# Kernel optimization log

Hardware: AMD Instinct MI355X
Metric: run time of the kernel (lower is better)

Reference implementation:

```python
import jax, jax.numpy as jnp
import numpy as np

D = 128          # embed_dim
NSYM = 100000    # num_symbols
PAD = NSYM       # padding idx (zero row)
B = 2048         # query batch
FEW = 5          # support set size
M = 128          # max neighbors
KTAB = 64        # knn table width
K = 32           # knn_k topk
STEPS = 4        # process_steps
DM = 2 * D       # d_model for encoders (256)
HID = 2 * DM     # LSTM hidden (512)


def _cos(a, b):
    # torch F.cosine_similarity, eps=1e-8; a [B,1,d], b [B,N,d] -> [B,N]
    num = jnp.sum(a * b, axis=-1)
    den = jnp.maximum(jnp.linalg.norm(a, axis=-1) * jnp.linalg.norm(b, axis=-1), 1e-8)
    return num / den


def _l2n(x):
    return x / jnp.maximum(jnp.linalg.norm(x, axis=-1, keepdims=True), 1e-12)


def _neighbor_encoder(conn, ids, knn_tab, emb, gcn_w, gcn_w_b, gcn_b, gate_w, gate_b):
    rel = emb[conn[..., 0]]                      # [N,M,D]
    ent = emb[conn[..., 1]]                      # [N,M,D]
    center = emb[ids][:, None, :]                # [N,1,D]
    sim = _cos(center, ent)                      # [N,M]
    _, idx = jax.lax.top_k(sim, K)               # [N,K]
    rel_k = jnp.take_along_axis(rel, idx[..., None], axis=1)
    ent_k = jnp.take_along_axis(ent, idx[..., None], axis=1)
    h = jnp.concatenate([rel_k, ent_k], axis=-1) @ gcn_w.T + gcn_w_b + gcn_b
    struct = jnp.tanh(h.mean(axis=1))            # [N,D]
    # knn branch: gather knn neighbor ids, cosine topk, pad-relation embeds (zero row)
    kent = emb[knn_tab[ids]]                     # [N,KTAB,D]
    sim2 = _cos(center, kent)
    _, idx2 = jax.lax.top_k(sim2, K)
    kent_k = jnp.take_along_axis(kent, idx2[..., None], axis=1)
    pad_row = jax.lax.stop_gradient(emb[PAD])    # padding_idx row (zeros, no grad)
    krel = jnp.broadcast_to(pad_row, kent_k.shape)
    h2 = jnp.concatenate([krel, kent_k], axis=-1) @ gcn_w.T + gcn_w_b + gcn_b
    knn_mean = jnp.tanh(h2.mean(axis=1))         # [N,D]
    alpha = jax.nn.sigmoid(jnp.concatenate([struct, knn_mean], axis=-1) @ gate_w.T + gate_b)
    return (1.0 - alpha) * struct + alpha * knn_mean


def _support_encoder(x, p1_w, p1_b, p2_w, p2_b, ln_g, ln_b):
    o = jax.nn.relu(x @ p1_w.T + p1_b) @ p2_w.T + p2_b
    z = o + x
    mu = z.mean(axis=-1, keepdims=True)
    sig = z.std(axis=-1, ddof=1, keepdims=True)  # torch unbiased std
    return (z - mu) / (sig + 1e-3) * ln_g + ln_b


def _query_encoder(support, query, w_ih, w_hh, b_ih, b_hh):
    # attLSTM processing block; support [1,DM], query [B,DM]
    n = query.shape[0]
    h_r = jnp.zeros((n, HID), query.dtype)
    c = jnp.zeros((n, HID), query.dtype)
    h = query
    for _ in range(STEPS):
        g = query @ w_ih.T + b_ih + h_r @ w_hh.T + b_hh
        i, f, gg, o = jnp.split(g, 4, axis=-1)
        c = jax.nn.sigmoid(f) * c + jax.nn.sigmoid(i) * jnp.tanh(gg)
        h_ = jax.nn.sigmoid(o) * jnp.tanh(c)
        h = query + h_[:, :DM]
        attn = jax.nn.softmax(h @ support.T, axis=1)  # [B,1]
        r = attn @ support                             # [B,DM]
        h_r = jnp.concatenate([h, r], axis=1)
    return h


def _forward(query, support, q_l_conn, q_r_conn, s_l_conn, s_r_conn, knn_neighbors,
             emb, gcn_w, gcn_w_b, gcn_b, gate_w, gate_b,
             p1_w, p1_b, p2_w, p2_b, ln_g, ln_b, w_ih, w_hh, b_ih, b_hh):
    ne = lambda conn, ids: _neighbor_encoder(conn, ids, knn_neighbors, emb,
                                             gcn_w, gcn_w_b, gcn_b, gate_w, gate_b)
    ql = ne(q_l_conn, query[:, 0])
    qr = ne(q_r_conn, query[:, 1])
    sl = ne(s_l_conn, support[:, 0])
    sr = ne(s_r_conn, support[:, 1])
    qn = jnp.concatenate([ql, qr], axis=-1)   # [B,DM]
    sn = jnp.concatenate([sl, sr], axis=-1)   # [FEW,DM]
    se = lambda x: _support_encoder(x, p1_w, p1_b, p2_w, p2_b, ln_g, ln_b)
    support_g = se(sn).mean(axis=0, keepdims=True)  # [1,DM]
    query_g = se(qn)                                 # [B,DM]
    query_f = _l2n(_query_encoder(support_g, query_g, w_ih, w_hh, b_ih, b_hh))
    sg = _l2n(support_g[0])
    return query_f @ sg                              # [B]


def setup_inputs() -> dict:
    key = jax.random.key(0)
    ks = jax.random.split(key, 24)
    f = lambda i, shape, s=0.05: jax.random.normal(ks[i], shape, dtype=jnp.float32) * s
    ri = lambda i, shape: jax.random.randint(ks[i], shape, 0, NSYM).astype(jnp.int32)
    emb = f(0, (NSYM + 1, D), 0.5).at[PAD].set(0.0)
    return dict(
        query=ri(1, (B, 2)), support=ri(2, (FEW, 2)),
        q_l_conn=ri(3, (B, M, 2)),
        q_l_deg=jax.random.randint(ks[4], (B,), 1, M).astype(jnp.int32),
        q_r_conn=ri(5, (B, M, 2)),
        q_r_deg=jax.random.randint(ks[6], (B,), 1, M).astype(jnp.int32),
        s_l_conn=ri(7, (FEW, M, 2)),
        s_l_deg=jax.random.randint(ks[8], (FEW,), 1, M).astype(jnp.int32),
        s_r_conn=ri(9, (FEW, M, 2)),
        s_r_deg=jax.random.randint(ks[10], (FEW,), 1, M).astype(jnp.int32),
        knn_neighbors=ri(11, (NSYM + 1, KTAB)),
        emb=emb,
        gcn_w=f(12, (D, 2 * D)), gcn_w_b=f(13, (D,)),
        gcn_b=jnp.zeros((D,), jnp.float32),
        gate_w=f(14, (1, 2 * D)), gate_b=jnp.zeros((1,), jnp.float32),
        p1_w=f(15, (2 * DM, DM)), p1_b=f(16, (2 * DM,)),
        p2_w=f(17, (DM, 2 * DM)), p2_b=f(18, (DM,)),
        ln_g=jnp.ones((DM,), jnp.float32), ln_b=jnp.zeros((DM,), jnp.float32),
        w_ih=f(19, (4 * HID, DM)), w_hh=f(20, (4 * HID, HID)),
        b_ih=f(21, (4 * HID,)), b_hh=f(22, (4 * HID,)),
    )


def reference(query, support, q_l_conn, q_l_deg, q_r_conn, q_r_deg,
              s_l_conn, s_l_deg, s_r_conn, s_r_deg, knn_neighbors,
              emb, gcn_w, gcn_w_b, gcn_b, gate_w, gate_b,
              p1_w, p1_b, p2_w, p2_b, ln_g, ln_b, w_ih, w_hh, b_ih, b_hh):
    # degrees are computed-but-unused in this fork's neighbor_encoder (plain mean)
    return _forward(query, support, q_l_conn, q_r_conn, s_l_conn, s_r_conn, knn_neighbors,
                    emb, gcn_w, gcn_w_b, gcn_b, gate_w, gate_b,
                    p1_w, p1_b, p2_w, p2_b, ln_g, ln_b, w_ih, w_hh, b_ih, b_hh)
```

## Files before the change

kernel.cpp:

```cpp
#include <hip/hip_runtime.h>
#include <hip/hip_bf16.h>

typedef unsigned short u16;
typedef unsigned int u32;

constexpr int ED   = 128;
constexpr int MC   = 128;
constexpr int KT   = 64;
constexpr int KS   = 32;
constexpr int NB   = 2048;
constexpr int NF   = 5;
constexpr int DMM  = 256;
constexpr int NG   = 1024;
constexpr int PADID = 100000;
constexpr int NROWS = 2*NB + 2*NF;
constexpr int MT   = (NROWS + 63)/64;
constexpr int MP   = MT*64;

typedef __attribute__((ext_vector_type(8))) short short8;
typedef __attribute__((ext_vector_type(4))) float floatx4;

__device__ __forceinline__ float bf2f(u16 u){
  union { u32 i; float f; } v; v.i = ((u32)u) << 16; return v.f;
}
__device__ __forceinline__ float lo2f(u32 w){
  union { u32 i; float f; } v; v.i = w << 16; return v.f;
}
__device__ __forceinline__ float hi2f(u32 w){
  union { u32 i; float f; } v; v.i = w & 0xffff0000u; return v.f;
}
__device__ __forceinline__ u16 f2bf(float f){
  union { float f; u32 i; } v; v.f = f;
  u32 r = v.i + 0x7FFFu + ((v.i >> 16) & 1u);
  return (u16)(r >> 16);
}
__device__ __forceinline__ float sigf(float x){ return 1.f / (1.f + expf(-x)); }

__device__ __forceinline__ float gld(const void* p, size_t i, bool bf){
  return bf ? bf2f(((const u16*)p)[i]) : ((const float*)p)[i];
}
__device__ __forceinline__ void ld2(const void* p, size_t i0, bool bf, float* o){
  if (bf){ u32 w = *(const u32*)((const u16*)p + i0); o[0]=lo2f(w); o[1]=hi2f(w); }
  else   { float2 v = *(const float2*)((const float*)p + i0); o[0]=v.x; o[1]=v.y; }
}
__device__ __forceinline__ void ld4(const void* p, size_t i0, bool bf, float* o){
  if (bf){ uint2 w = *(const uint2*)((const u16*)p + i0);
           o[0]=lo2f(w.x); o[1]=hi2f(w.x); o[2]=lo2f(w.y); o[3]=hi2f(w.y); }
  else   { float4 v = *(const float4*)((const float*)p + i0);
           o[0]=v.x; o[1]=v.y; o[2]=v.z; o[3]=v.w; }
}
__device__ __forceinline__ void ld8(const void* p, size_t i0, bool bf, float* o){
  if (bf){
    uint4 v = *(const uint4*)((const u16*)p + i0);
    o[0]=lo2f(v.x); o[1]=hi2f(v.x); o[2]=lo2f(v.y); o[3]=hi2f(v.y);
    o[4]=lo2f(v.z); o[5]=hi2f(v.z); o[6]=lo2f(v.w); o[7]=hi2f(v.w);
  } else {
    const float* f = (const float*)p + i0;
    float4 a = *(const float4*)f, b = *(const float4*)(f + 4);
    o[0]=a.x; o[1]=a.y; o[2]=a.z; o[3]=a.w; o[4]=b.x; o[5]=b.y; o[6]=b.z; o[7]=b.w;
  }
}
__device__ __forceinline__ float dotw(const void* w, size_t i0, const float* x, int n, bool bf){
  float acc = 0.f, t[8];
  #pragma unroll 4
  for (int j = 0; j < n; j += 8){
    ld8(w, i0 + j, bf, t);
    #pragma unroll
    for (int q = 0; q < 8; q++) acc += t[q]*x[j+q];
  }
  return acc;
}

__device__ __forceinline__ float waveSum(float v){
  #pragma unroll
  for (int o = 32; o > 0; o >>= 1) v += __shfl_xor(v, o, 64);
  return v;
}
__device__ __forceinline__ float blockSum(float v, float* s8){
  int lane = threadIdx.x & 63, wid = threadIdx.x >> 6;
  v = waveSum(v);
  __syncthreads();
  if (lane == 0) s8[wid] = v;
  __syncthreads();
  return s8[0] + s8[1] + s8[2] + s8[3];
}
__device__ __forceinline__ float2 blockSum2(float a, float b, float* s8){
  int lane = threadIdx.x & 63, wid = threadIdx.x >> 6;
  a = waveSum(a); b = waveSum(b);
  __syncthreads();
  if (lane == 0){ s8[wid] = a; s8[4 + wid] = b; }
  __syncthreads();
  float2 r;
  r.x = s8[0] + s8[1] + s8[2] + s8[3];
  r.y = s8[4] + s8[5] + s8[6] + s8[7];
  return r;
}

__global__ void sniff_kernel(const void* ln_g, int* flag){
  if (threadIdx.x == 0 && blockIdx.x == 0)
    *flag = (*(const u32*)ln_g == 0x3F803F80u) ? 1 : 0;
}

__global__ __launch_bounds__(256) void neighbor_kernel(
    const int* __restrict__ query, const int* __restrict__ support,
    const int* __restrict__ qlc, const int* __restrict__ qrc,
    const int* __restrict__ slc, const int* __restrict__ srcc,
    const int* __restrict__ knnt, const void* __restrict__ emb,
    float* __restrict__ gA, float* __restrict__ gK, const int* __restrict__ flag)
{
  const bool bf = (*flag != 0);
  int blk = blockIdx.x;
  const int* conn; int id;
  if (blk < NB)            { id = query[2*blk];                 conn = qlc + (size_t)blk*MC*2; }
  else if (blk < 2*NB)     { int r = blk - NB;   id = query[2*r+1];   conn = qrc + (size_t)r*MC*2; }
  else if (blk < 2*NB+NF)  { int r = blk - 2*NB; id = support[2*r];   conn = slc + (size_t)r*MC*2; }
  else                     { int r = blk - 2*NB - NF; id = support[2*r+1]; conn = srcc + (size_t)r*MC*2; }

  __shared__ float s_center[ED];
  __shared__ float s_sim[MC + KT];
  __shared__ float s_red[8];
  __shared__ int s_eid[MC + KT];
  __shared__ int s_selE[KS], s_selR[KS], s_selK[KS];
  __shared__ float s_mt[3][8][ED];

  const int tid = threadIdx.x, lane = tid & 63, wid = tid >> 6;

  if (tid < ED) s_center[tid] = gld(emb, (size_t)id*ED + tid, bf);
  if (tid < MC)           s_eid[tid] = conn[2*tid + 1];
  else if (tid < MC + KT) s_eid[tid] = knnt[(size_t)id*KT + (tid - MC)];

  float cpart = 0.f;
  if (tid < ED){ float c = s_center[tid]; cpart = c*c; }
  float cnorm = sqrtf(blockSum(cpart, s_red));

  const int g = lane & 15;
  float creg[8];
  #pragma unroll
  for (int j = 0; j < 8; j++) creg[j] = s_center[g*8 + j];

  #pragma unroll 4
  for (int m0 = wid*4; m0 < MC + KT; m0 += 16){
    int m = m0 + (lane >> 4);
    int eid = s_eid[m];
    float e[8];
    ld8(emb, (size_t)eid*ED + g*8, bf, e);
    float d = 0.f, q = 0.f;
    #pragma unroll
    for (int j = 0; j < 8; j++){ d += creg[j]*e[j]; q += e[j]*e[j]; }
    #pragma unroll
    for (int o = 8; o > 0; o >>= 1){ d += __shfl_xor(d, o, 64); q += __shfl_xor(q, o, 64); }
    if (g == 0) s_sim[m] = d / fmaxf(cnorm * sqrtf(q), 1e-8f);
  }
  __syncthreads();

  if (tid < MC){
    float v = s_sim[tid];
    int cnt = 0;
    #pragma unroll 8
    for (int j = 0; j < MC; j++){
      float w = s_sim[j];
      cnt += (w > v || (w == v && j < tid)) ? 1 : 0;
    }
    if (cnt < KS){ s_selR[cnt] = conn[2*tid]; s_selE[cnt] = s_eid[tid]; }
  } else if (tid < MC + KT){
    int t = tid - MC;
    float v = s_sim[MC + t];
    int cnt = 0;
    #pragma unroll 8
    for (int j = 0; j < KT; j++){
      float w = s_sim[MC + j];
      cnt += (w > v || (w == v && j < t)) ? 1 : 0;
    }
    if (cnt < KS) s_selK[cnt] = s_eid[MC + t];
  }
  __syncthreads();

  {
    const int slot = tid >> 5, c4 = (tid & 31)*4;
    float aR[4] = {0,0,0,0}, aE[4] = {0,0,0,0}, aK[4] = {0,0,0,0};
    #pragma unroll
    for (int k = 0; k < 4; k++){
      float t[4];
      ld4(emb, (size_t)s_selR[k*8 + slot]*ED + c4, bf, t);
      aR[0]+=t[0]; aR[1]+=t[1]; aR[2]+=t[2]; aR[3]+=t[3];
      ld4(emb, (size_t)s_selE[k*8 + slot]*ED + c4, bf, t);
      aE[0]+=t[0]; aE[1]+=t[1]; aE[2]+=t[2]; aE[3]+=t[3];
      ld4(emb, (size_t)s_selK[k*8 + slot]*ED + c4, bf, t);
      aK[0]+=t[0]; aK[1]+=t[1]; aK[2]+=t[2]; aK[3]+=t[3];
    }
    *(float4*)&s_mt[0][slot][c4] = make_float4(aR[0], aR[1], aR[2], aR[3]);
    *(float4*)&s_mt[1][slot][c4] = make_float4(aE[0], aE[1], aE[2], aE[3]);
    *(float4*)&s_mt[2][slot][c4] = make_float4(aK[0], aK[1], aK[2], aK[3]);
  }
  __syncthreads();
  {
    int dd = tid & (ED - 1), which = tid >> 7;
    float s = 0.f;
    #pragma unroll
    for (int p = 0; p < 8; p++) s += s_mt[which][p][dd];
    gA[(size_t)blk*DMM + which*ED + dd] = s * (1.f/KS);
    if (tid < ED){
      float sk = 0.f;
      #pragma unroll
      for (int p = 0; p < 8; p++) sk += s_mt[2][p][dd];
      gK[(size_t)blk*ED + dd] = sk * (1.f/KS);
    }
  }
}

__global__ __launch_bounds__(256) void gcn_gemm(
    const float* __restrict__ ARE, const float* __restrict__ AK,
    const void* __restrict__ gcn_w, const void* __restrict__ gcn_w_b,
    const void* __restrict__ gcn_b, float* __restrict__ C, const int* __restrict__ flag)
{
  const bool bf = (*flag != 0);
  __shared__ float As2[16][68];
  __shared__ float Ws2[16][68];
  int tid = threadIdx.x;
  int n0 = blockIdx.x * 64;
  int mt = blockIdx.y;
  const float* A; int lda, K, woff; size_t cbase; int mtt;
  if (mt < MT){ A = ARE; lda = DMM; K = DMM; woff = 0;  cbase = 0;              mtt = mt; }
  else        { A = AK;  lda = ED;  K = ED;  woff = ED; cbase = (size_t)MP*ED;  mtt = mt - MT; }
  int m0 = mtt*64;

  int tx = tid & 15, ty = tid >> 4;
  int sn_ = tid & 63, kq = tid >> 6;
  size_t wbase = (size_t)(n0 + sn_)*DMM + woff;
  int ar = tid >> 2, ac = (tid & 3)*4;
  const float* ap = A + (size_t)(m0 + ar)*lda + ac;

  float acc[4][4];
  #pragma unroll
  for (int i = 0; i < 4; i++)
    #pragma unroll
    for (int j = 0; j < 4; j++) acc[i][j] = 0.f;

  for (int kc = 0; kc < K; kc += 16){
    __syncthreads();
    float4 av = *(const float4*)(ap + kc);
    As2[ac+0][ar] = av.x; As2[ac+1][ar] = av.y; As2[ac+2][ar] = av.z; As2[ac+3][ar] = av.w;
    float wt[4];
    ld4(gcn_w, wbase + kc + kq*4, bf, wt);
    Ws2[kq*4+0][sn_] = wt[0]; Ws2[kq*4+1][sn_] = wt[1];
    Ws2[kq*4+2][sn_] = wt[2]; Ws2[kq*4+3][sn_] = wt[3];
    __syncthreads();
    #pragma unroll
    for (int k = 0; k < 16; k++){
      float4 a = *(const float4*)&As2[k][ty*4];
      float4 b = *(const float4*)&Ws2[k][tx*4];
      acc[0][0] += a.x*b.x; acc[0][1] += a.x*b.y; acc[0][2] += a.x*b.z; acc[0][3] += a.x*b.w;
      acc[1][0] += a.y*b.x; acc[1][1] += a.y*b.y; acc[1][2] += a.y*b.z; acc[1][3] += a.y*b.w;
      acc[2][0] += a.z*b.x; acc[2][1] += a.z*b.y; acc[2][2] += a.z*b.z; acc[2][3] += a.z*b.w;
      acc[3][0] += a.w*b.x; acc[3][1] += a.w*b.y; acc[3][2] += a.w*b.z; acc[3][3] += a.w*b.w;
    }
  }

  float b4[4];
  #pragma unroll
  for (int j = 0; j < 4; j++){
    int n = n0 + tx*4 + j;
    b4[j] = gld(gcn_w_b, n, bf) + gld(gcn_b, n, bf);
  }
  #pragma unroll
  for (int i = 0; i < 4; i++){
    int row = m0 + ty*4 + i;
    float4 v = make_float4(acc[i][0]+b4[0], acc[i][1]+b4[1], acc[i][2]+b4[2], acc[i][3]+b4[3]);
    *(float4*)(C + cbase + (size_t)row*ED + n0 + tx*4) = v;
  }
}

__global__ __launch_bounds__(256) void gcn_epilogue(
    const float* __restrict__ C, const void* __restrict__ gate_w,
    const void* __restrict__ gate_b, float* __restrict__ qn,
    float* __restrict__ sn, const int* __restrict__ flag)
{
  const bool bf = (*flag != 0);
  int wv = threadIdx.x >> 6, lane = threadIdx.x & 63;
  int r = blockIdx.x*4 + wv;
  if (r >= NROWS) return;
  const float* c1 = C + (size_t)r*ED;
  const float* c2 = C + (size_t)(MP + r)*ED;
  float2 sv = *(const float2*)(c1 + 2*lane);
  float2 kv = *(const float2*)(c2 + 2*lane);
  float s0 = tanhf(sv.x), s1 = tanhf(sv.y);
  float k0 = tanhf(kv.x), k1 = tanhf(kv.y);
  float gv = gld(gate_w, 2*lane, bf)*s0 + gld(gate_w, 2*lane+1, bf)*s1
           + gld(gate_w, ED + 2*lane, bf)*k0 + gld(gate_w, ED + 2*lane+1, bf)*k1;
  gv = waveSum(gv);
  float alpha = sigf(gv + gld(gate_b, 0, bf));
  float* outp;
  if (r < NB)             outp = qn + (size_t)r*DMM;
  else if (r < 2*NB)      outp = qn + (size_t)(r - NB)*DMM + ED;
  else if (r < 2*NB + NF) outp = sn + (size_t)(r - 2*NB)*DMM;
  else                    outp = sn + (size_t)(r - 2*NB - NF)*DMM + ED;
  float2 o;
  o.x = (1.f - alpha)*s0 + alpha*k0;
  o.y = (1.f - alpha)*s1 + alpha*k1;
  *(float2*)(outp + 2*lane) = o;
}

__global__ __launch_bounds__(256) void mlp_enc_kernel(
    const float* __restrict__ src,
    const void* __restrict__ p1_w, const void* __restrict__ p1_b,
    const void* __restrict__ p2_w, const void* __restrict__ p2_b,
    const void* __restrict__ ln_g, const void* __restrict__ ln_b,
    float* __restrict__ dst, int nrows, const int* __restrict__ flag)
{
  const bool bf = (*flag != 0);
  constexpr int RPB = 8;
  __shared__ float x[RPB][DMM];
  __shared__ float hid[RPB][2*DMM];
  __shared__ float s_red[8];
  int tid = threadIdx.x;
  int r0 = blockIdx.x * RPB;
  for (int r = 0; r < RPB; r++)
    x[r][tid] = (r0 + r < nrows) ? src[(size_t)(r0 + r)*DMM + tid] : 0.f;
  __syncthreads();

  {
    float acc0[RPB], acc1[RPB];
    #pragma unroll
    for (int r = 0; r < RPB; r++){ acc0[r] = 0.f; acc1[r] = 0.f; }
    for (int j8 = 0; j8 < DMM/8; j8++){
      float wa[8], wb[8];
      ld8(p1_w, (size_t)tid*DMM + j8*8, bf, wa);
      ld8(p1_w, (size_t)(tid+256)*DMM + j8*8, bf, wb);
      #pragma unroll
      for (int r = 0; r < RPB; r++){
        const float* xr = &x[r][j8*8];
        float s0 = 0.f, s1 = 0.f;
        #pragma unroll
        for (int q = 0; q < 8; q++){ float xv = xr[q]; s0 += wa[q]*xv; s1 += wb[q]*xv; }
        acc0[r] += s0; acc1[r] += s1;
      }
    }
    float bb0 = gld(p1_b, tid, bf), bb1 = gld(p1_b, tid + 256, bf);
    #pragma unroll
    for (int r = 0; r < RPB; r++){
      hid[r][tid]     = fmaxf(acc0[r] + bb0, 0.f);
      hid[r][tid+256] = fmaxf(acc1[r] + bb1, 0.f);
    }
  }
  __syncthreads();

  float zr[RPB];
  {
    #pragma unroll
    for (int r = 0; r < RPB; r++) zr[r] = 0.f;
    for (int j8 = 0; j8 < (2*DMM)/8; j8++){
      float wa[8];
      ld8(p2_w, (size_t)tid*(2*DMM) + j8*8, bf, wa);
      #pragma unroll
      for (int r = 0; r < RPB; r++){
        const float* hr = &hid[r][j8*8];
        float s0 = 0.f;
        #pragma unroll
        for (int q = 0; q < 8; q++) s0 += wa[q]*hr[q];
        zr[r] += s0;
      }
    }
    float bb = gld(p2_b, tid, bf);
    #pragma unroll
    for (int r = 0; r < RPB; r++) zr[r] += bb + x[r][tid];
  }

  float lg = gld(ln_g, tid, bf), lb = gld(ln_b, tid, bf);
  for (int r = 0; r < RPB; r++){
    float2 st = blockSum2(zr[r], zr[r]*zr[r], s_red);
    float mu = st.x * (1.f/DMM);
    float var = (st.y - (float)DMM*mu*mu) * (1.f/(DMM - 1));
    float sig = sqrtf(fmaxf(var, 0.f));
    if (r0 + r < nrows)
      dst[(size_t)(r0 + r)*DMM + tid] = (zr[r] - mu)/(sig + 1e-3f)*lg + lb;
  }
}

__global__ __launch_bounds__(256) void svec_kernel(
    const void* __restrict__ w_hh, const void* __restrict__ b_ih, const void* __restrict__ b_hh,
    const float* __restrict__ seS, float* __restrict__ cvec0, float* __restrict__ svec,
    float* __restrict__ sgn, const int* __restrict__ flag)
{
  const bool bf = (*flag != 0);
  __shared__ float sg[DMM];
  __shared__ float s_red[8];
  int tid = threadIdx.x;
  float a = 0.f;
  for (int r = 0; r < NF; r++) a += seS[r*DMM + tid];
  a *= (1.f/NF);
  sg[tid] = a;
  __syncthreads();
  if (blockIdx.x == 0){
    float nn = blockSum(a*a, s_red);
    sgn[tid] = a / fmaxf(sqrtf(nn), 1e-12f);
  }
  int u = blockIdx.x * 256 + tid;
  int wrow = (u >> 8)*512 + (u & 255);
  cvec0[u] = gld(b_ih, wrow, bf) + gld(b_hh, wrow, bf);
  svec[u] = dotw(w_hh, (size_t)wrow*(2*DMM) + DMM, sg, DMM, bf);
}

__global__ __launch_bounds__(256) void gemm_gates(
    const float* __restrict__ A,
    const void* __restrict__ W, int wstride,
    const float* __restrict__ addvec, const float* __restrict__ addmat,
    float* __restrict__ C, const int* __restrict__ flag)
{
  const bool bf = (*flag != 0);
  int tid = threadIdx.x;
  int n0 = blockIdx.x * 64, m0 = blockIdx.y * 64;

  if (bf){
    constexpr int KP = 136;
    __shared__ u16 As[64 * KP];
    __shared__ u16 Ws[64 * KP];
    const int wv = tid >> 6, lane = tid & 63;
    const int quad = lane >> 4, l16 = lane & 15;
    const int sr = tid >> 5, sc = tid & 31;

    floatx4 acc[4];
    #pragma unroll
    for (int t = 0; t < 4; t++) acc[t] = (floatx4){0.f, 0.f, 0.f, 0.f};

    for (int kc = 0; kc < 256; kc += 128){
      __syncthreads();
      #pragma unroll
      for (int i = 0; i < 8; i++){
        int r = i*8 + sr;
        float4 v = *(const float4*)(A + (size_t)(m0 + r)*256 + kc + sc*4);
        u32 p0 = (u32)f2bf(v.x) | ((u32)f2bf(v.y) << 16);
        u32 p1 = (u32)f2bf(v.z) | ((u32)f2bf(v.w) << 16);
        *(uint2*)&As[r*KP + sc*4] = make_uint2(p0, p1);
      }
      #pragma unroll
      for (int i = 0; i < 8; i++){
        int nn = i*8 + sr;
        int gn = n0 + nn;
        int wrow = (gn >> 8)*512 + (gn & 255);
        uint2 wv2 = *(const uint2*)((const u16*)W + (size_t)wrow*wstride + kc + sc*4);
        *(uint2*)&Ws[nn*KP + sc*4] = wv2;
      }
      __syncthreads();
      int am = wv*16 + l16;
      #pragma unroll
      for (int k1 = 0; k1 < 128; k1 += 32){
        int ko = k1 + quad*8;
        short8 af = *(const short8*)&As[am*KP + ko];
        #pragma unroll
        for (int t = 0; t < 4; t++){
          short8 bfr = *(const short8*)&Ws[(t*16 + l16)*KP + ko];
          acc[t] = __builtin_amdgcn_mfma_f32_16x16x32_bf16(af, bfr, acc[t], 0, 0, 0);
        }
      }
    }

    #pragma unroll
    for (int t = 0; t < 4; t++){
      int col = n0 + t*16 + l16;
      float av = addvec ? addvec[col] : 0.f;
      #pragma unroll
      for (int r = 0; r < 4; r++){
        int row = m0 + wv*16 + quad*4 + r;
        float val = acc[t][r] + av;
        if (addmat) val += addmat[(size_t)row*NG + col];
        C[(size_t)row*NG + col] = val;
      }
    }
    return;
  }

  {
    __shared__ float As2[16][68];
    __shared__ float Ws2[16][68];
    int tx = tid & 15, ty = tid >> 4;
    int sn_ = tid & 63, kq = tid >> 6;
    int gn = n0 + sn_;
    size_t wbase = (size_t)((gn >> 8)*512 + (gn & 255)) * wstride;
    int ar = tid >> 2, ac = (tid & 3) * 4;
    const float* ap = A + (size_t)(m0 + ar)*256 + ac;

    float acc[4][4];
    #pragma unroll
    for (int i = 0; i < 4; i++)
      #pragma unroll
      for (int j = 0; j < 4; j++) acc[i][j] = 0.f;

    for (int kc = 0; kc < 256; kc += 16){
      __syncthreads();
      float4 av = *(const float4*)(ap + kc);
      As2[ac+0][ar] = av.x; As2[ac+1][ar] = av.y; As2[ac+2][ar] = av.z; As2[ac+3][ar] = av.w;
      float wt[4];
      ld4(W, wbase + kc + kq*4, false, wt);
      Ws2[kq*4+0][sn_] = wt[0]; Ws2[kq*4+1][sn_] = wt[1];
      Ws2[kq*4+2][sn_] = wt[2]; Ws2[kq*4+3][sn_] = wt[3];
      __syncthreads();
      #pragma unroll
      for (int k = 0; k < 16; k++){
        float4 a = *(const float4*)&As2[k][ty*4];
        float4 b = *(const float4*)&Ws2[k][tx*4];
        acc[0][0] += a.x*b.x; acc[0][1] += a.x*b.y; acc[0][2] += a.x*b.z; acc[0][3] += a.x*b.w;
        acc[1][0] += a.y*b.x; acc[1][1] += a.y*b.y; acc[1][2] += a.y*b.z; acc[1][3] += a.y*b.w;
        acc[2][0] += a.z*b.x; acc[2][1] += a.z*b.y; acc[2][2] += a.z*b.z; acc[2][3] += a.z*b.w;
        acc[3][0] += a.w*b.x; acc[3][1] += a.w*b.y; acc[3][2] += a.w*b.z; acc[3][3] += a.w*b.w;
      }
    }

    float4 addc = make_float4(0.f, 0.f, 0.f, 0.f);
    if (addvec){
      float4 t = *(const float4*)(addvec + n0 + tx*4);
      addc.x = t.x; addc.y = t.y; addc.z = t.z; addc.w = t.w;
    }
    #pragma unroll
    for (int i = 0; i < 4; i++){
      int row = m0 + ty*4 + i;
      float4 v = make_float4(acc[i][0]+addc.x, acc[i][1]+addc.y, acc[i][2]+addc.z, acc[i][3]+addc.w);
      if (addmat){
        float4 t = *(const float4*)(addmat + (size_t)row*NG + n0 + tx*4);
        v.x += t.x; v.y += t.y; v.z += t.z; v.w += t.w;
      }
      *(float4*)(C + (size_t)row*NG + n0 + tx*4) = v;
    }
  }
}

__global__ __launch_bounds__(256) void lstm_elem(
    const float* __restrict__ g, const float* __restrict__ query_g,
    float* __restrict__ c, float* __restrict__ h, int first,
    const float* __restrict__ sgn, void* __restrict__ out, const int* __restrict__ flag)
{
  __shared__ float s_red[8];
  int b = blockIdx.x, j = threadIdx.x;
  const float* gb = g + (size_t)b*NG;
  float iv = gb[j], fv = gb[256 + j], gv = gb[512 + j], ov = gb[768 + j];
  float cc = first ? 0.f : c[(size_t)b*DMM + j];
  cc = sigf(fv)*cc + sigf(iv)*tanhf(gv);
  c[(size_t)b*DMM + j] = cc;
  float hh = query_g[(size_t)b*DMM + j] + sigf(ov)*tanhf(cc);
  h[(size_t)b*DMM + j] = hh;
  if (out){
    float2 st = blockSum2(hh*sgn[j], hh*hh, s_red);
    if (j == 0){
      float v = st.x / fmaxf(sqrtf(st.y), 1e-12f);
      if (*flag) ((__hip_bfloat16*)out)[b] = __float2bfloat16(v);
      else       ((float*)out)[b] = v;
    }
  }
}

extern "C" void kernel_launch(void* const* d_in, const int* in_sizes, int n_in,
                              void* d_out, int out_size, void* d_ws, size_t ws_size,
                              hipStream_t stream)
{
  const int* query   = (const int*)d_in[0];
  const int* support = (const int*)d_in[1];
  const int* qlc     = (const int*)d_in[2];
  const int* qrc     = (const int*)d_in[4];
  const int* slc     = (const int*)d_in[6];
  const int* srcc    = (const int*)d_in[8];
  const int* knnt    = (const int*)d_in[10];
  const void* emb     = d_in[11];
  const void* gcn_w   = d_in[12];
  const void* gcn_w_b = d_in[13];
  const void* gcn_b   = d_in[14];
  const void* gate_w  = d_in[15];
  const void* gate_b  = d_in[16];
  const void* p1_w    = d_in[17];
  const void* p1_b    = d_in[18];
  const void* p2_w    = d_in[19];
  const void* p2_b    = d_in[20];
  const void* ln_g    = d_in[21];
  const void* ln_b    = d_in[22];
  const void* w_ih    = d_in[23];
  const void* w_hh    = d_in[24];
  const void* b_ih    = d_in[25];
  const void* b_hh    = d_in[26];

  int* flag = (int*)d_ws;
  float* ws = (float*)d_ws + 64;
  size_t off = 0;
  float* qn        = ws + off; off += (size_t)NB*DMM;
  float* sn        = ws + off; off += NF*DMM;
  float* query_g   = ws + off; off += (size_t)NB*DMM;
  float* seS       = ws + off; off += NF*DMM;
  float* sgn       = ws + off; off += DMM;
  float* cvec0     = ws + off; off += NG;
  float* svec      = ws + off; off += NG;
  float* qx        = ws + off; off += (size_t)NB*NG;
  float* gbuf      = ws + off; off += (size_t)NB*NG;
  float* hbuf      = ws + off; off += (size_t)NB*DMM;
  float* cbuf      = ws + off; off += (size_t)NB*DMM;
  float* gA        = ws + off; off += (size_t)MP*DMM;
  float* gK        = ws + off; off += (size_t)MP*ED;
  float* gC        = ws + off; off += (size_t)2*MP*ED;
  (void)sn; (void)seS;

  sniff_kernel<<<1, 64, 0, stream>>>(ln_g, flag);

  neighbor_kernel<<<NROWS, 256, 0, stream>>>(
      query, support, qlc, qrc, slc, srcc, knnt, emb, gA, gK, flag);

  gcn_gemm<<<dim3(2, 2*MT), 256, 0, stream>>>(gA, gK, gcn_w, gcn_w_b, gcn_b, gC, flag);

  gcn_epilogue<<<(NROWS + 3)/4, 256, 0, stream>>>(gC, gate_w, gate_b, qn, sn, flag);

  mlp_enc_kernel<<<(NB + NF + 7)/8, 256, 0, stream>>>(
      qn, p1_w, p1_b, p2_w, p2_b, ln_g, ln_b, query_g, NB + NF, flag);

  svec_kernel<<<NG/256, 256, 0, stream>>>(w_hh, b_ih, b_hh, seS, cvec0, svec, sgn, flag);

  gemm_gates<<<dim3(NG/64, NB/64), 256, 0, stream>>>(query_g, w_ih, 256, cvec0, nullptr, qx, flag);

  lstm_elem<<<NB, 256, 0, stream>>>(qx, query_g, cbuf, hbuf, 1, nullptr, nullptr, flag);
  for (int s = 1; s < 4; s++){
    gemm_gates<<<dim3(NG/64, NB/64), 256, 0, stream>>>(hbuf, w_hh, 512, svec, qx, gbuf, flag);
    lstm_elem<<<NB, 256, 0, stream>>>(gbuf, query_g, cbuf, hbuf, 0,
                                      sgn, (s == 3) ? d_out : nullptr, flag);
  }

  (void)in_sizes; (void)n_in; (void)out_size; (void)ws_size;
}
```

Measured before the change: 434.1 us.

## Fuse LSTM steps into one persistent kernel with transposed fp32 weights

Replaces the per-step gate GEMM and elementwise LSTM launches with a single kernel. Each block keeps 8 rows of hidden and cell state in shared memory and registers across all four steps, reading fp32 weights that a prep kernel transposes first. This removes the round trips of the gate, h and c buffers through global memory and several kernel launches, and the separate sniff kernel is replaced by an inline dtype check in each kernel. In exchange the bf16 MFMA path is dropped for scalar fp32 FMAs, and each block re-reads the full weight matrices from cache.

```diff
diff --git a/kernel.cpp b/kernel.cpp
--- a/kernel.cpp
+++ b/kernel.cpp
@@ -17,9 +17,6 @@
 constexpr int MT   = (NROWS + 63)/64;
 constexpr int MP   = MT*64;
 
-typedef __attribute__((ext_vector_type(8))) short short8;
-typedef __attribute__((ext_vector_type(4))) float floatx4;
-
 __device__ __forceinline__ float bf2f(u16 u){
   union { u32 i; float f; } v; v.i = ((u32)u) << 16; return v.f;
 }
@@ -29,19 +26,14 @@
 __device__ __forceinline__ float hi2f(u32 w){
   union { u32 i; float f; } v; v.i = w & 0xffff0000u; return v.f;
 }
-__device__ __forceinline__ u16 f2bf(float f){
-  union { float f; u32 i; } v; v.f = f;
-  u32 r = v.i + 0x7FFFu + ((v.i >> 16) & 1u);
-  return (u16)(r >> 16);
-}
 __device__ __forceinline__ float sigf(float x){ return 1.f / (1.f + expf(-x)); }
+
+__device__ __forceinline__ bool sniff(const void* ln_g){
+  return *(const u32*)ln_g == 0x3F803F80u;
+}
 
 __device__ __forceinline__ float gld(const void* p, size_t i, bool bf){
   return bf ? bf2f(((const u16*)p)[i]) : ((const float*)p)[i];
-}
-__device__ __forceinline__ void ld2(const void* p, size_t i0, bool bf, float* o){
-  if (bf){ u32 w = *(const u32*)((const u16*)p + i0); o[0]=lo2f(w); o[1]=hi2f(w); }
-  else   { float2 v = *(const float2*)((const float*)p + i0); o[0]=v.x; o[1]=v.y; }
 }
 __device__ __forceinline__ void ld4(const void* p, size_t i0, bool bf, float* o){
   if (bf){ uint2 w = *(const uint2*)((const u16*)p + i0);
@@ -60,16 +52,6 @@
     o[0]=a.x; o[1]=a.y; o[2]=a.z; o[3]=a.w; o[4]=b.x; o[5]=b.y; o[6]=b.z; o[7]=b.w;
   }
 }
-__device__ __forceinline__ float dotw(const void* w, size_t i0, const float* x, int n, bool bf){
-  float acc = 0.f, t[8];
-  #pragma unroll 4
-  for (int j = 0; j < n; j += 8){
-    ld8(w, i0 + j, bf, t);
-    #pragma unroll
-    for (int q = 0; q < 8; q++) acc += t[q]*x[j+q];
-  }
-  return acc;
-}
 
 __device__ __forceinline__ float waveSum(float v){
   #pragma unroll
@@ -94,11 +76,6 @@
   r.x = s8[0] + s8[1] + s8[2] + s8[3];
   r.y = s8[4] + s8[5] + s8[6] + s8[7];
   return r;
-}
-
-__global__ void sniff_kernel(const void* ln_g, int* flag){
-  if (threadIdx.x == 0 && blockIdx.x == 0)
-    *flag = (*(const u32*)ln_g == 0x3F803F80u) ? 1 : 0;
 }
 
 __global__ __launch_bounds__(256) void neighbor_kernel(
@@ -106,9 +83,9 @@
     const int* __restrict__ qlc, const int* __restrict__ qrc,
     const int* __restrict__ slc, const int* __restrict__ srcc,
     const int* __restrict__ knnt, const void* __restrict__ emb,
-    float* __restrict__ gA, float* __restrict__ gK, const int* __restrict__ flag)
+    float* __restrict__ gA, float* __restrict__ gK, const void* __restrict__ ln_g)
 {
-  const bool bf = (*flag != 0);
+  const bool bf = sniff(ln_g);
   int blk = blockIdx.x;
   const int* conn; int id;
   if (blk < NB)            { id = query[2*blk];                 conn = qlc + (size_t)blk*MC*2; }
@@ -211,9 +188,9 @@
 __global__ __launch_bounds__(256) void gcn_gemm(
     const float* __restrict__ ARE, const float* __restrict__ AK,
     const void* __restrict__ gcn_w, const void* __restrict__ gcn_w_b,
-    const void* __restrict__ gcn_b, float* __restrict__ C, const int* __restrict__ flag)
+    const void* __restrict__ gcn_b, float* __restrict__ C, const void* __restrict__ ln_g)
 {
-  const bool bf = (*flag != 0);
+  const bool bf = sniff(ln_g);
   __shared__ float As2[16][68];
   __shared__ float Ws2[16][68];
   int tid = threadIdx.x;
@@ -273,9 +250,9 @@
 __global__ __launch_bounds__(256) void gcn_epilogue(
     const float* __restrict__ C, const void* __restrict__ gate_w,
     const void* __restrict__ gate_b, float* __restrict__ qn,
-    float* __restrict__ sn, const int* __restrict__ flag)
+    float* __restrict__ sn, const void* __restrict__ ln_g)
 {
-  const bool bf = (*flag != 0);
+  const bool bf = sniff(ln_g);
   int wv = threadIdx.x >> 6, lane = threadIdx.x & 63;
   int r = blockIdx.x*4 + wv;
   if (r >= NROWS) return;
@@ -305,9 +282,9 @@
     const void* __restrict__ p1_w, const void* __restrict__ p1_b,
     const void* __restrict__ p2_w, const void* __restrict__ p2_b,
     const void* __restrict__ ln_g, const void* __restrict__ ln_b,
-    float* __restrict__ dst, int nrows, const int* __restrict__ flag)
+    float* __restrict__ dst, int nrows)
 {
-  const bool bf = (*flag != 0);
+  const bool bf = sniff(ln_g);
   constexpr int RPB = 8;
   __shared__ float x[RPB][DMM];
   __shared__ float hid[RPB][2*DMM];
@@ -376,173 +353,229 @@
   }
 }
 
-__global__ __launch_bounds__(256) void svec_kernel(
-    const void* __restrict__ w_hh, const void* __restrict__ b_ih, const void* __restrict__ b_hh,
-    const float* __restrict__ seS, float* __restrict__ cvec0, float* __restrict__ svec,
-    float* __restrict__ sgn, const int* __restrict__ flag)
+__global__ __launch_bounds__(256) void prep_kernel(
+    const void* __restrict__ w_ih, const void* __restrict__ w_hh,
+    const void* __restrict__ b_ih, const void* __restrict__ b_hh,
+    const float* __restrict__ seS,
+    float* __restrict__ WT_ih, float* __restrict__ WT_hh,
+    float* __restrict__ svec, float* __restrict__ cvec0,
+    float* __restrict__ sgn, const void* __restrict__ ln_g)
 {
-  const bool bf = (*flag != 0);
-  __shared__ float sg[DMM];
-  __shared__ float s_red[8];
-  int tid = threadIdx.x;
-  float a = 0.f;
-  for (int r = 0; r < NF; r++) a += seS[r*DMM + tid];
-  a *= (1.f/NF);
-  sg[tid] = a;
-  __syncthreads();
-  if (blockIdx.x == 0){
-    float nn = blockSum(a*a, s_red);
-    sgn[tid] = a / fmaxf(sqrtf(nn), 1e-12f);
-  }
-  int u = blockIdx.x * 256 + tid;
-  int wrow = (u >> 8)*512 + (u & 255);
-  cvec0[u] = gld(b_ih, wrow, bf) + gld(b_hh, wrow, bf);
-  svec[u] = dotw(w_hh, (size_t)wrow*(2*DMM) + DMM, sg, DMM, bf);
-}
-
-__global__ __launch_bounds__(256) void gemm_gates(
-    const float* __restrict__ A,
-    const void* __restrict__ W, int wstride,
-    const float* __restrict__ addvec, const float* __restrict__ addmat,
-    float* __restrict__ C, const int* __restrict__ flag)
+  const bool bf = sniff(ln_g);
+  const int b = blockIdx.x, tid = threadIdx.x;
+  if (b < 32){
+    const void* W = (b < 16) ? w_ih : w_hh;
+    const int wstride = (b < 16) ? 256 : 512;
+    float* WT = (b < 16) ? WT_ih : WT_hh;
+    const int n0 = (b & 15) * 64;
+    __shared__ float tile[64][65];
+    const int nl = tid >> 2, kq = tid & 3;
+    const int kl = tid >> 2, nq = tid & 3;
+    const int wrow = ((n0 + nl) >> 8)*512 + ((n0 + nl) & 255);
+    for (int kc = 0; kc < 256; kc += 64){
+      __syncthreads();
+      float t[16];
+      ld8(W, (size_t)wrow*wstride + kc + kq*16,     bf, t);
+      ld8(W, (size_t)wrow*wstride + kc + kq*16 + 8, bf, t + 8);
+      #pragma unroll
+      for (int i = 0; i < 16; i++) tile[nl][kq*16 + i] = t[i];
+      __syncthreads();
+      float o[16];
+      #pragma unroll
+      for (int i = 0; i < 16; i++) o[i] = tile[nq*16 + i][kl];
+      #pragma unroll
+      for (int i = 0; i < 16; i += 4)
+        *(float4*)&WT[(size_t)(kc + kl)*NG + n0 + nq*16 + i] =
+            make_float4(o[i], o[i+1], o[i+2], o[i+3]);
+    }
+  } else {
+    const int n0 = (b - 32) * 64;
+    __shared__ float sg[DMM];
+    __shared__ float part[64][4];
+    __shared__ float s_red[8];
+    if (tid < DMM){
+      float a = 0.f;
+      #pragma unroll
+      for (int r = 0; r < NF; r++) a += seS[r*DMM + tid];
+      sg[tid] = a * (1.f/NF);
+    }
+    __syncthreads();
+    if (b == 32){
+      float sq = (tid < DMM) ? sg[tid]*sg[tid] : 0.f;
+      float nn = blockSum(sq, s_red);
+      if (tid < DMM) sgn[tid] = sg[tid] / fmaxf(sqrtf(nn), 1e-12f);
+    }
+    const int nl = tid >> 2, q = tid & 3;
+    const int n = n0 + nl;
+    const int wrow = (n >> 8)*512 + (n & 255);
+    float acc = 0.f, t[8];
+    #pragma unroll
+    for (int k8 = 0; k8 < 8; k8++){
+      ld8(w_hh, (size_t)wrow*(2*DMM) + DMM + q*64 + k8*8, bf, t);
+      #pragma unroll
+      for (int j = 0; j < 8; j++) acc += t[j]*sg[q*64 + k8*8 + j];
+    }
+    part[nl][q] = acc;
+    __syncthreads();
+    if (tid < 64){
+      svec[n0 + tid] = part[tid][0] + part[tid][1] + part[tid][2] + part[tid][3];
+      const int wr2 = ((n0 + tid) >> 8)*512 + ((n0 + tid) & 255);
+      cvec0[n0 + tid] = gld(b_ih, wr2, bf) + gld(b_hh, wr2, bf);
+    }
+  }
+}
+
+__global__ __launch_bounds__(256) void fused_lstm(
+    const float* __restrict__ query_g,
+    const float* __restrict__ WT_ih, const float* __restrict__ WT_hh,
+    const float* __restrict__ svec, const float* __restrict__ cvec0,
+    const float* __restrict__ sgn_g, const void* __restrict__ ln_g,
+    void* __restrict__ out)
 {
-  const bool bf = (*flag != 0);
-  int tid = threadIdx.x;
-  int n0 = blockIdx.x * 64, m0 = blockIdx.y * 64;
-
-  if (bf){
-    constexpr int KP = 136;
-    __shared__ u16 As[64 * KP];
-    __shared__ u16 Ws[64 * KP];
-    const int wv = tid >> 6, lane = tid & 63;
-    const int quad = lane >> 4, l16 = lane & 15;
-    const int sr = tid >> 5, sc = tid & 31;
-
-    floatx4 acc[4];
-    #pragma unroll
-    for (int t = 0; t < 4; t++) acc[t] = (floatx4){0.f, 0.f, 0.f, 0.f};
-
-    for (int kc = 0; kc < 256; kc += 128){
+  const bool bf = sniff(ln_g);
+  const int tid = threadIdx.x;
+  const int m0 = blockIdx.x * 8;
+  const int jj0 = (tid & 63) * 4;
+  const int rg = tid >> 6;
+  const int r0 = rg * 2;
+
+  __shared__ float s_qg[8][260];
+  __shared__ float s_h[8][260];
+  __shared__ float s_sgn[DMM];
+
+  {
+    int r = tid >> 5, c8 = (tid & 31) * 8;
+    const float* src = query_g + (size_t)(m0 + r)*DMM + c8;
+    float4 v0 = *(const float4*)src, v1 = *(const float4*)(src + 4);
+    *(float4*)&s_qg[r][c8]   = v0;  *(float4*)&s_qg[r][c8+4] = v1;
+    *(float4*)&s_h[r][c8]    = v0;  *(float4*)&s_h[r][c8+4]  = v1;
+  }
+  s_sgn[tid] = sgn_g[tid];
+  float4 sv[4], cv[4];
+  #pragma unroll
+  for (int g = 0; g < 4; g++){
+    sv[g] = *(const float4*)&svec[g*256 + jj0];
+    cv[g] = *(const float4*)&cvec0[g*256 + jj0];
+  }
+  __syncthreads();
+
+  float qx[2][4][4];
+  {
+    float acc[2][4][4];
+    #pragma unroll
+    for (int r = 0; r < 2; r++)
+      #pragma unroll
+      for (int g = 0; g < 4; g++)
+        #pragma unroll
+        for (int j = 0; j < 4; j++) acc[r][g][j] = 0.f;
+    #pragma unroll 4
+    for (int k = 0; k < 256; k++){
+      float a0 = s_h[r0][k], a1 = s_h[r0+1][k];
+      const float* wr = WT_ih + (size_t)k*NG + jj0;
+      float w[4][4];
+      *(float4*)&w[0][0] = *(const float4*)(wr);
+      *(float4*)&w[1][0] = *(const float4*)(wr + 256);
+      *(float4*)&w[2][0] = *(const float4*)(wr + 512);
+      *(float4*)&w[3][0] = *(const float4*)(wr + 768);
+      #pragma unroll
+      for (int g = 0; g < 4; g++)
+        #pragma unroll
+        for (int j = 0; j < 4; j++){
+          acc[0][g][j] += a0 * w[g][j];
+          acc[1][g][j] += a1 * w[g][j];
+        }
+    }
+    #pragma unroll
+    for (int r = 0; r < 2; r++)
+      #pragma unroll
+      for (int g = 0; g < 4; g++){
+        qx[r][g][0] = acc[r][g][0] + cv[g].x;
+        qx[r][g][1] = acc[r][g][1] + cv[g].y;
+        qx[r][g][2] = acc[r][g][2] + cv[g].z;
+        qx[r][g][3] = acc[r][g][3] + cv[g].w;
+      }
+  }
+
+  float cst[2][4];
+  #pragma unroll
+  for (int r = 0; r < 2; r++)
+    #pragma unroll
+    for (int j = 0; j < 4; j++) cst[r][j] = 0.f;
+  float hreg[2][4];
+
+  for (int s = 0; s < 4; s++){
+    float gacc[2][4][4];
+    if (s == 0){
+      #pragma unroll
+      for (int r = 0; r < 2; r++)
+        #pragma unroll
+        for (int g = 0; g < 4; g++)
+          #pragma unroll
+          for (int j = 0; j < 4; j++) gacc[r][g][j] = qx[r][g][j];
+    } else {
+      #pragma unroll
+      for (int r = 0; r < 2; r++)
+        #pragma unroll
+        for (int g = 0; g < 4; g++){
+          gacc[r][g][0] = qx[r][g][0] + sv[g].x;
+          gacc[r][g][1] = qx[r][g][1] + sv[g].y;
+          gacc[r][g][2] = qx[r][g][2] + sv[g].z;
+          gacc[r][g][3] = qx[r][g][3] + sv[g].w;
+        }
+      #pragma unroll 4
+      for (int k = 0; k < 256; k++){
+        float a0 = s_h[r0][k], a1 = s_h[r0+1][k];
+        const float* wr = WT_hh + (size_t)k*NG + jj0;
+        float w[4][4];
+        *(float4*)&w[0][0] = *(const float4*)(wr);
+        *(float4*)&w[1][0] = *(const float4*)(wr + 256);
+        *(float4*)&w[2][0] = *(const float4*)(wr + 512);
+        *(float4*)&w[3][0] = *(const float4*)(wr + 768);
+        #pragma unroll
+        for (int g = 0; g < 4; g++)
+          #pragma unroll
+          for (int j = 0; j < 4; j++){
+            gacc[0][g][j] += a0 * w[g][j];
+            gacc[1][g][j] += a1 * w[g][j];
+          }
+      }
+    }
+    #pragma unroll
+    for (int r = 0; r < 2; r++)
+      #pragma unroll
+      for (int j = 0; j < 4; j++){
+        float iv = gacc[r][0][j], fv = gacc[r][1][j];
+        float gv = gacc[r][2][j], ov = gacc[r][3][j];
+        float cc = sigf(fv)*cst[r][j] + sigf(iv)*tanhf(gv);
+        cst[r][j] = cc;
+        hreg[r][j] = s_qg[r0 + r][jj0 + j] + sigf(ov)*tanhf(cc);
+      }
+    __syncthreads();
+    if (s < 3){
+      *(float4*)&s_h[r0][jj0]   = make_float4(hreg[0][0], hreg[0][1], hreg[0][2], hreg[0][3]);
+      *(float4*)&s_h[r0+1][jj0] = make_float4(hreg[1][0], hreg[1][1], hreg[1][2], hreg[1][3]);
       __syncthreads();
-      #pragma unroll
-      for (int i = 0; i < 8; i++){
-        int r = i*8 + sr;
-        float4 v = *(const float4*)(A + (size_t)(m0 + r)*256 + kc + sc*4);
-        u32 p0 = (u32)f2bf(v.x) | ((u32)f2bf(v.y) << 16);
-        u32 p1 = (u32)f2bf(v.z) | ((u32)f2bf(v.w) << 16);
-        *(uint2*)&As[r*KP + sc*4] = make_uint2(p0, p1);
-      }
-      #pragma unroll
-      for (int i = 0; i < 8; i++){
-        int nn = i*8 + sr;
-        int gn = n0 + nn;
-        int wrow = (gn >> 8)*512 + (gn & 255);
-        uint2 wv2 = *(const uint2*)((const u16*)W + (size_t)wrow*wstride + kc + sc*4);
-        *(uint2*)&Ws[nn*KP + sc*4] = wv2;
-      }
-      __syncthreads();
-      int am = wv*16 + l16;
-      #pragma unroll
-      for (int k1 = 0; k1 < 128; k1 += 32){
-        int ko = k1 + quad*8;
-        short8 af = *(const short8*)&As[am*KP + ko];
-        #pragma unroll
-        for (int t = 0; t < 4; t++){
-          short8 bfr = *(const short8*)&Ws[(t*16 + l16)*KP + ko];
-          acc[t] = __builtin_amdgcn_mfma_f32_16x16x32_bf16(af, bfr, acc[t], 0, 0, 0);
-        }
-      }
-    }
-
-    #pragma unroll
-    for (int t = 0; t < 4; t++){
-      int col = n0 + t*16 + l16;
-      float av = addvec ? addvec[col] : 0.f;
-      #pragma unroll
-      for (int r = 0; r < 4; r++){
-        int row = m0 + wv*16 + quad*4 + r;
-        float val = acc[t][r] + av;
-        if (addmat) val += addmat[(size_t)row*NG + col];
-        C[(size_t)row*NG + col] = val;
-      }
-    }
-    return;
-  }
-
-  {
-    __shared__ float As2[16][68];
-    __shared__ float Ws2[16][68];
-    int tx = tid & 15, ty = tid >> 4;
-    int sn_ = tid & 63, kq = tid >> 6;
-    int gn = n0 + sn_;
-    size_t wbase = (size_t)((gn >> 8)*512 + (gn & 255)) * wstride;
-    int ar = tid >> 2, ac = (tid & 3) * 4;
-    const float* ap = A + (size_t)(m0 + ar)*256 + ac;
-
-    float acc[4][4];
-    #pragma unroll
-    for (int i = 0; i < 4; i++)
-      #pragma unroll
-      for (int j = 0; j < 4; j++) acc[i][j] = 0.f;
-
-    for (int kc = 0; kc < 256; kc += 16){
-      __syncthreads();
-      float4 av = *(const float4*)(ap + kc);
-      As2[ac+0][ar] = av.x; As2[ac+1][ar] = av.y; As2[ac+2][ar] = av.z; As2[ac+3][ar] = av.w;
-      float wt[4];
-      ld4(W, wbase + kc + kq*4, false, wt);
-      Ws2[kq*4+0][sn_] = wt[0]; Ws2[kq*4+1][sn_] = wt[1];
-      Ws2[kq*4+2][sn_] = wt[2]; Ws2[kq*4+3][sn_] = wt[3];
-      __syncthreads();
-      #pragma unroll
-      for (int k = 0; k < 16; k++){
-        float4 a = *(const float4*)&As2[k][ty*4];
-        float4 b = *(const float4*)&Ws2[k][tx*4];
-        acc[0][0] += a.x*b.x; acc[0][1] += a.x*b.y; acc[0][2] += a.x*b.z; acc[0][3] += a.x*b.w;
-        acc[1][0] += a.y*b.x; acc[1][1] += a.y*b.y; acc[1][2] += a.y*b.z; acc[1][3] += a.y*b.w;
-        acc[2][0] += a.z*b.x; acc[2][1] += a.z*b.y; acc[2][2] += a.z*b.z; acc[2][3] += a.z*b.w;
-        acc[3][0] += a.w*b.x; acc[3][1] += a.w*b.y; acc[3][2] += a.w*b.z; acc[3][3] += a.w*b.w;
-      }
-    }
-
-    float4 addc = make_float4(0.f, 0.f, 0.f, 0.f);
-    if (addvec){
-      float4 t = *(const float4*)(addvec + n0 + tx*4);
-      addc.x = t.x; addc.y = t.y; addc.z = t.z; addc.w = t.w;
-    }
-    #pragma unroll
-    for (int i = 0; i < 4; i++){
-      int row = m0 + ty*4 + i;
-      float4 v = make_float4(acc[i][0]+addc.x, acc[i][1]+addc.y, acc[i][2]+addc.z, acc[i][3]+addc.w);
-      if (addmat){
-        float4 t = *(const float4*)(addmat + (size_t)row*NG + n0 + tx*4);
-        v.x += t.x; v.y += t.y; v.z += t.z; v.w += t.w;
-      }
-      *(float4*)(C + (size_t)row*NG + n0 + tx*4) = v;
-    }
-  }
-}
-
-__global__ __launch_bounds__(256) void lstm_elem(
-    const float* __restrict__ g, const float* __restrict__ query_g,
-    float* __restrict__ c, float* __restrict__ h, int first,
-    const float* __restrict__ sgn, void* __restrict__ out, const int* __restrict__ flag)
-{
-  __shared__ float s_red[8];
-  int b = blockIdx.x, j = threadIdx.x;
-  const float* gb = g + (size_t)b*NG;
-  float iv = gb[j], fv = gb[256 + j], gv = gb[512 + j], ov = gb[768 + j];
-  float cc = first ? 0.f : c[(size_t)b*DMM + j];
-  cc = sigf(fv)*cc + sigf(iv)*tanhf(gv);
-  c[(size_t)b*DMM + j] = cc;
-  float hh = query_g[(size_t)b*DMM + j] + sigf(ov)*tanhf(cc);
-  h[(size_t)b*DMM + j] = hh;
-  if (out){
-    float2 st = blockSum2(hh*sgn[j], hh*hh, s_red);
-    if (j == 0){
-      float v = st.x / fmaxf(sqrtf(st.y), 1e-12f);
-      if (*flag) ((__hip_bfloat16*)out)[b] = __float2bfloat16(v);
-      else       ((float*)out)[b] = v;
+    }
+  }
+
+  float d0 = 0.f, q0 = 0.f, d1 = 0.f, q1 = 0.f;
+  #pragma unroll
+  for (int j = 0; j < 4; j++){
+    float g0 = s_sgn[jj0 + j];
+    d0 += hreg[0][j]*g0; q0 += hreg[0][j]*hreg[0][j];
+    d1 += hreg[1][j]*g0; q1 += hreg[1][j]*hreg[1][j];
+  }
+  d0 = waveSum(d0); q0 = waveSum(q0);
+  d1 = waveSum(d1); q1 = waveSum(q1);
+  if ((tid & 63) == 0){
+    float v0 = d0 / fmaxf(sqrtf(q0), 1e-12f);
+    float v1 = d1 / fmaxf(sqrtf(q1), 1e-12f);
+    if (bf){
+      ((__hip_bfloat16*)out)[m0 + r0]     = __float2bfloat16(v0);
+      ((__hip_bfloat16*)out)[m0 + r0 + 1] = __float2bfloat16(v1);
+    } else {
+      ((float*)out)[m0 + r0]     = v0;
+      ((float*)out)[m0 + r0 + 1] = v1;
     }
   }
 }
@@ -575,47 +608,37 @@
   const void* b_ih    = d_in[25];
   const void* b_hh    = d_in[26];
 
-  int* flag = (int*)d_ws;
   float* ws = (float*)d_ws + 64;
   size_t off = 0;
-  float* qn        = ws + off; off += (size_t)NB*DMM;
-  float* sn        = ws + off; off += NF*DMM;
-  float* query_g   = ws + off; off += (size_t)NB*DMM;
-  float* seS       = ws + off; off += NF*DMM;
-  float* sgn       = ws + off; off += DMM;
-  float* cvec0     = ws + off; off += NG;
-  float* svec      = ws + off; off += NG;
-  float* qx        = ws + off; off += (size_t)NB*NG;
-  float* gbuf      = ws + off; off += (size_t)NB*NG;
-  float* hbuf      = ws + off; off += (size_t)NB*DMM;
-  float* cbuf      = ws + off; off += (size_t)NB*DMM;
-  float* gA        = ws + off; off += (size_t)MP*DMM;
-  float* gK        = ws + off; off += (size_t)MP*ED;
-  float* gC        = ws + off; off += (size_t)2*MP*ED;
-  (void)sn; (void)seS;
-
-  sniff_kernel<<<1, 64, 0, stream>>>(ln_g, flag);
+  float* qn      = ws + off; off += (size_t)NB*DMM;
+  float* sn      = ws + off; off += NF*DMM;
+  float* query_g = ws + off; off += (size_t)NB*DMM;
+  float* seS     = ws + off; off += NF*DMM;
+  float* sgn     = ws + off; off += DMM;
+  float* cvec0   = ws + off; off += NG;
+  float* svec    = ws + off; off += NG;
+  float* WT_ih   = ws + off; off += (size_t)DMM*NG;
+  float* WT_hh   = ws + off; off += (size_t)DMM*NG;
+  float* gA      = ws + off; off += (size_t)MP*DMM;
+  float* gK      = ws + off; off += (size_t)MP*ED;
+  float* gC      = ws + off; off += (size_t)2*MP*ED;
+  (void)sn;
 
   neighbor_kernel<<<NROWS, 256, 0, stream>>>(
-      query, support, qlc, qrc, slc, srcc, knnt, emb, gA, gK, flag);
-
-  gcn_gemm<<<dim3(2, 2*MT), 256, 0, stream>>>(gA, gK, gcn_w, gcn_w_b, gcn_b, gC, flag);
-
-  gcn_epilogue<<<(NROWS + 3)/4, 256, 0, stream>>>(gC, gate_w, gate_b, qn, sn, flag);
+      query, support, qlc, qrc, slc, srcc, knnt, emb, gA, gK, ln_g);
+
+  gcn_gemm<<<dim3(2, 2*MT), 256, 0, stream>>>(gA, gK, gcn_w, gcn_w_b, gcn_b, gC, ln_g);
+
+  gcn_epilogue<<<(NROWS + 3)/4, 256, 0, stream>>>(gC, gate_w, gate_b, qn, sn, ln_g);
 
   mlp_enc_kernel<<<(NB + NF + 7)/8, 256, 0, stream>>>(
-      qn, p1_w, p1_b, p2_w, p2_b, ln_g, ln_b, query_g, NB + NF, flag);
-
-  svec_kernel<<<NG/256, 256, 0, stream>>>(w_hh, b_ih, b_hh, seS, cvec0, svec, sgn, flag);
-
-  gemm_gates<<<dim3(NG/64, NB/64), 256, 0, stream>>>(query_g, w_ih, 256, cvec0, nullptr, qx, flag);
-
-  lstm_elem<<<NB, 256, 0, stream>>>(qx, query_g, cbuf, hbuf, 1, nullptr, nullptr, flag);
-  for (int s = 1; s < 4; s++){
-    gemm_gates<<<dim3(NG/64, NB/64), 256, 0, stream>>>(hbuf, w_hh, 512, svec, qx, gbuf, flag);
-    lstm_elem<<<NB, 256, 0, stream>>>(gbuf, query_g, cbuf, hbuf, 0,
-                                      sgn, (s == 3) ? d_out : nullptr, flag);
-  }
+      qn, p1_w, p1_b, p2_w, p2_b, ln_g, ln_b, query_g, NB + NF);
+
+  prep_kernel<<<48, 256, 0, stream>>>(
+      w_ih, w_hh, b_ih, b_hh, seS, WT_ih, WT_hh, svec, cvec0, sgn, ln_g);
+
+  fused_lstm<<<NB/8, 256, 0, stream>>>(
+      query_g, WT_ih, WT_hh, svec, cvec0, sgn, ln_g, d_out);
 
   (void)in_sizes; (void)n_in; (void)out_size; (void)ws_size;
 }
```

New measurement: 827.6 us. 90.6% more time.
